# Performance work log

Measured on AMD Instinct MI355X. Metric: run time of the kernel, lower is better.

## Reference

```python
import jax, jax.numpy as jnp
import numpy as np

N = 100000      # nodes
E = 1600000     # edges (avg degree 16)
F_IN = 128      # num_features
H = 64          # hidden_dim
C = 7           # num_classes


def setup_inputs() -> dict:
    key = jax.random.key(0)
    ks = jax.random.split(key, 9)
    x = jax.random.normal(ks[0], (N, F_IN), dtype=jnp.float32)
    edge_index = jax.random.randint(ks[1], (2, E), 0, N, dtype=jnp.int32)
    s1 = 1.0 / np.sqrt(F_IN)
    s2 = 1.0 / np.sqrt(H)
    # SAGEConv1: lin_l applied to aggregated neighbors, lin_r to root
    W1l = jax.random.uniform(ks[2], (F_IN, H), jnp.float32, -s1, s1)
    W1r = jax.random.uniform(ks[3], (F_IN, H), jnp.float32, -s1, s1)
    b1 = jax.random.uniform(ks[4], (H,), jnp.float32, -s1, s1)
    # SAGEConv2
    W2l = jax.random.uniform(ks[5], (H, C), jnp.float32, -s2, s2)
    W2r = jax.random.uniform(ks[6], (H, C), jnp.float32, -s2, s2)
    b2 = jax.random.uniform(ks[7], (C,), jnp.float32, -s2, s2)
    return {"x": x, "edge_index": edge_index, "W1l": W1l, "W1r": W1r,
            "b1": b1, "W2l": W2l, "W2r": W2r, "b2": b2}


def _segment_mean(vals, idx, num_segments):
    # scatter-mean: sum messages per destination node, divide by in-degree
    sums = jax.ops.segment_sum(vals, idx, num_segments=num_segments)
    cnt = jax.ops.segment_sum(jnp.ones(idx.shape, vals.dtype), idx,
                              num_segments=num_segments)
    return sums / jnp.maximum(cnt, 1.0)[:, None]


def reference(x, edge_index, W1l, W1r, b1, W2l, W2r, b2):
    src, dst = edge_index[0], edge_index[1]
    # SAGEConv 1: mean of neighbor (src) features at each dst, plus root term
    agg1 = _segment_mean(x[src], dst, N)              # [N, F_IN]
    h = agg1 @ W1l + x @ W1r + b1                     # [N, H]
    h = jax.nn.relu(h)
    # dropout is inactive in eval mode (deterministic reference)
    # SAGEConv 2
    agg2 = _segment_mean(h[src], dst, N)              # [N, H]
    out = agg2 @ W2l + h @ W2r + b2                   # [N, C]
    return jax.nn.log_softmax(out, axis=1)
```

## Files before the change

### kernel.cpp

```cpp
#include <hip/hip_runtime.h>
#include <cstdint>
#include <cstddef>


#define CAP 64
#define BINSZ 128
#define CH 4096

typedef __attribute__((ext_vector_type(8))) short bf16x8v;
typedef __attribute__((ext_vector_type(4))) float f32x4v;
typedef __attribute__((ext_vector_type(2))) unsigned int u32x2v;

__device__ __forceinline__ float bf2f(unsigned short u) {
  return __uint_as_float(((unsigned int)u) << 16);
}
__device__ __forceinline__ unsigned short f2bf(float f) {
  unsigned int x = __float_as_uint(f);
  unsigned int r = (x + 0x7fffu + ((x >> 16) & 1u)) >> 16;
  return (unsigned short)r;
}

__device__ __forceinline__ float swap16_add(float x) {
  u32x2v p = __builtin_amdgcn_permlane16_swap(__float_as_uint(x), __float_as_uint(x), false, false);
  return __uint_as_float(p[0]) + __uint_as_float(p[1]);
}
__device__ __forceinline__ float swap32_add(float x) {
  u32x2v p = __builtin_amdgcn_permlane32_swap(__float_as_uint(x), __float_as_uint(x), false, false);
  return __uint_as_float(p[0]) + __uint_as_float(p[1]);
}

#define DPP_ROR_ADD(x, CTRL)                                                  \
  (x) = (x) + __int_as_float(__builtin_amdgcn_update_dpp(                     \
            __float_as_int(x), __float_as_int(x), (CTRL), 0xF, 0xF, false))

__global__ __launch_bounds__(256) void k_hist(const int* __restrict__ ei,
                                              int* __restrict__ hist,
                                              const float* __restrict__ W1l,
                                              const float* __restrict__ W1r,
                                              unsigned short* __restrict__ wswz,
                                              int* __restrict__ cursor,
                                              int E, int NB, int NCH) {
  const int t = threadIdx.x;
  if (blockIdx.x >= (unsigned)NCH) {
    if (blockIdx.x == (unsigned)NCH && t == 0) *cursor = 0;
    int idx = (blockIdx.x - NCH) * 256 + t;
    int j = idx & 7;
    int lane = (idx >> 3) & 63;
    int c = (idx >> 9) & 7;
    int t4 = idx >> 12;
    int kk = t4 * 32 + (lane >> 4) * 8 + j;
    int nn = c * 16 + (lane & 15);
    float v = (nn < 64) ? W1l[kk * 64 + nn] : W1r[kk * 64 + (nn - 64)];
    wswz[idx] = f2bf(v);
    return;
  }
  __shared__ int lcnt[1024];
  const int c = blockIdx.x;
  for (int i = t; i < NB; i += 256) lcnt[i] = 0;
  __syncthreads();
  const int base = c * CH;
  const int end = min(base + CH, E);
  for (int e = base + t; e < end; e += 256) {
    int d = ei[E + e];
    atomicAdd(&lcnt[d >> 7], 1);
  }
  __syncthreads();
  for (int i = t; i < NB; i += 256) hist[(size_t)i * NCH + c] = lcnt[i];
}

__global__ __launch_bounds__(256) void k_scan_gemm(
    int* __restrict__ hist, int* __restrict__ tot, int* __restrict__ binbase,
    int* __restrict__ cursor, int NB, int NCH, int nScan,
    const float* __restrict__ x, const unsigned short* __restrict__ wswz,
    const float* __restrict__ b1, unsigned short* __restrict__ xl,
    unsigned short* __restrict__ hroot, int Nn) {
  if (blockIdx.x < (unsigned)nScan) {
    const int lane = threadIdx.x & 63;
    const int bin = blockIdx.x * 4 + (threadIdx.x >> 6);
    if (bin >= NB) return;
    int* h = hist + (size_t)bin * NCH;
    int carry = 0;
    for (int base = 0; base < NCH; base += 64) {
      int i = base + lane;
      int v = (i < NCH) ? h[i] : 0;
      int incl = v;
      #pragma unroll
      for (int d = 1; d < 64; d <<= 1) {
        int t = __shfl_up(incl, d, 64);
        if (lane >= d) incl += t;
      }
      if (i < NCH) h[i] = carry + incl - v;
      carry += __shfl(incl, 63, 64);
    }
    if (lane == 0) {
      tot[bin] = carry;
      binbase[bin] = atomicAdd(cursor, carry);
    }
    return;
  }
  __shared__ unsigned short Bsw[16384];
  const int t = threadIdx.x;
  const int bid = blockIdx.x - nScan;
  {
    const uint4* src = (const uint4*)wswz;
    uint4* dst = (uint4*)Bsw;
    #pragma unroll
    for (int i = 0; i < 8; ++i) dst[t + i * 256] = src[t + i * 256];
  }
  __syncthreads();

  const int lane = t & 63;
  const int wid = t >> 6;
  const int quad = lane >> 4;
  const int m = lane & 15;
  const int rowA = bid * 64 + wid * 16 + m;
  const float* xrow = x + (size_t)min(rowA, Nn - 1) * 128;

  f32x4v acc[8];
  #pragma unroll
  for (int c = 0; c < 8; ++c) acc[c] = (f32x4v){0.f, 0.f, 0.f, 0.f};

  #pragma unroll
  for (int t4 = 0; t4 < 4; ++t4) {
    const int koff = t4 * 32 + quad * 8;
    float4 a0 = *(const float4*)(xrow + koff);
    float4 a1 = *(const float4*)(xrow + koff + 4);
    bf16x8v af;
    af[0] = (short)f2bf(a0.x); af[1] = (short)f2bf(a0.y);
    af[2] = (short)f2bf(a0.z); af[3] = (short)f2bf(a0.w);
    af[4] = (short)f2bf(a1.x); af[5] = (short)f2bf(a1.y);
    af[6] = (short)f2bf(a1.z); af[7] = (short)f2bf(a1.w);
    #pragma unroll
    for (int c = 0; c < 8; ++c) {
      const bf16x8v bf_ = *(const bf16x8v*)&Bsw[(((t4 * 8 + c) * 64 + lane)) << 3];
      acc[c] = __builtin_amdgcn_mfma_f32_16x16x32_bf16(af, bf_, acc[c], 0, 0, 0);
    }
  }

  const int rbase = bid * 64 + wid * 16 + quad * 4;
  #pragma unroll
  for (int c = 0; c < 8; ++c) {
    const int col = c * 16 + m;
    #pragma unroll
    for (int i = 0; i < 4; ++i) {
      const int r = rbase + i;
      if (r < Nn) {
        if (c < 4) xl[(size_t)r * 64 + col] = f2bf(acc[c][i]);
        else       hroot[(size_t)r * 64 + (col - 64)] = f2bf(acc[c][i] + b1[col - 64]);
      }
    }
  }
}

__global__ __launch_bounds__(256) void k_scat(const int* __restrict__ ei,
                                              const int* __restrict__ hist,
                                              const int* __restrict__ binbase,
                                              unsigned int* __restrict__ part,
                                              int E, int NB, int NCH) {
  __shared__ int lcur[1024];
  const int c = blockIdx.x, t = threadIdx.x;
  for (int i = t; i < NB; i += 256)
    lcur[i] = hist[(size_t)i * NCH + c] + binbase[i];
  __syncthreads();
  const int base = c * CH;
  const int end = min(base + CH, E);
  for (int e = base + t; e < end; e += 256) {
    int s = ei[e];
    int d = ei[E + e];
    int bin = d >> 7;
    int pos = atomicAdd(&lcur[bin], 1);
    part[pos] = (unsigned)s | ((unsigned)(d & 127) << 17);
  }
}

__global__ __launch_bounds__(256) void k_bucketB(const int* __restrict__ binbase,
                                                 const int* __restrict__ tot,
                                                 const unsigned int* __restrict__ part,
                                                 int* __restrict__ cnt,
                                                 int* __restrict__ bucket) {
  __shared__ int lbkt[BINSZ * CAP];
  __shared__ int ldeg[BINSZ];
  const int b = blockIdx.x, t = threadIdx.x;
  if (t < BINSZ) ldeg[t] = 0;
  __syncthreads();
  const int e0 = binbase[b], e1 = e0 + tot[b];
  for (int i = e0 + t; i < e1; i += 256) {
    unsigned rec = part[i];
    int loc = rec >> 17;
    int p = atomicAdd(&ldeg[loc], 1);
    if (p < CAP) lbkt[loc * CAP + p] = (int)(rec & 0x1FFFFu);
  }
  __syncthreads();
  if (t < BINSZ) cnt[b * BINSZ + t] = ldeg[t];
  const int4* s4 = (const int4*)lbkt;
  int4* d4 = (int4*)(bucket + (size_t)b * BINSZ * CAP);
  #pragma unroll 2
  for (int i = t; i < BINSZ * CAP / 4; i += 256) d4[i] = s4[i];
}

__global__ __launch_bounds__(256) void k_agg1(
    const int* __restrict__ cnt, const int* __restrict__ bucket,
    const unsigned int* __restrict__ xl32, const unsigned int* __restrict__ hroot32,
    const float* __restrict__ W2l, const float* __restrict__ W2r,
    const float* __restrict__ b2,
    float* __restrict__ hl, float* __restrict__ hr, int Nn) {
  const int lane = threadIdx.x & 63;
  const int q = lane & 15;
  const unsigned qo = 2u * q;
  const int g = lane >> 4;
  const int nw = gridDim.x * (blockDim.x >> 6);
  int n = blockIdx.x * (blockDim.x >> 6) + (threadIdx.x >> 6);
  if (n >= Nn) return;

  float wreg[4][4];
  float bcr[4];
  #pragma unroll
  for (int k = 0; k < 4; ++k) {
    const int o = (g << 2) + k;
    bcr[k] = (o >= 8 && o < 15) ? b2[o - 8] : 0.f;
    #pragma unroll
    for (int j = 0; j < 4; ++j) {
      const int kk = (q << 2) + j;
      float wv = 0.f;
      if (o < 7)                 wv = W2l[kk * 7 + o];
      else if (o >= 8 && o < 15) wv = W2r[kk * 7 + (o - 8)];
      wreg[j][k] = wv;
    }
  }

  int c  = cnt[n];
  int c1 = cnt[min(n + nw, Nn - 1)];
  int m = c < CAP ? c : CAP;
  int sidx = (lane < m) ? bucket[((unsigned)n << 6) + lane] : 0;
  if ((unsigned)sidx >= (unsigned)Nn) sidx = 0;
  uint2 hu = *(const uint2*)(hroot32 + ((unsigned)n << 5) + qo);

  while (true) {
    const int n1 = n + nw;
    const int n1c = min(n1, Nn - 1);
    const int m1 = c1 < CAP ? c1 : CAP;
    int sidx1 = (lane < m1) ? bucket[((unsigned)n1c << 6) + lane] : 0;
    uint2 hu1 = *(const uint2*)(hroot32 + ((unsigned)n1c << 5) + qo);
    int c2 = cnt[min(n1 + nw, Nn - 1)];

    float a0 = 0.f, a1 = 0.f, a2 = 0.f, a3 = 0.f;
    int i = 0;
    for (; i + 16 <= m; i += 16) {
      int rA = __shfl(sidx, i + g, 64);
      int rB = __shfl(sidx, i + 4 + g, 64);
      int rC = __shfl(sidx, i + 8 + g, 64);
      int rD = __shfl(sidx, i + 12 + g, 64);
      uint2 uA = *(const uint2*)(xl32 + (((unsigned)rA) << 5) + qo);
      uint2 uB = *(const uint2*)(xl32 + (((unsigned)rB) << 5) + qo);
      uint2 uC = *(const uint2*)(xl32 + (((unsigned)rC) << 5) + qo);
      uint2 uD = *(const uint2*)(xl32 + (((unsigned)rD) << 5) + qo);
      a0 += (__uint_as_float(uA.x << 16) + __uint_as_float(uB.x << 16))
          + (__uint_as_float(uC.x << 16) + __uint_as_float(uD.x << 16));
      a1 += (__uint_as_float(uA.x & 0xFFFF0000u) + __uint_as_float(uB.x & 0xFFFF0000u))
          + (__uint_as_float(uC.x & 0xFFFF0000u) + __uint_as_float(uD.x & 0xFFFF0000u));
      a2 += (__uint_as_float(uA.y << 16) + __uint_as_float(uB.y << 16))
          + (__uint_as_float(uC.y << 16) + __uint_as_float(uD.y << 16));
      a3 += (__uint_as_float(uA.y & 0xFFFF0000u) + __uint_as_float(uB.y & 0xFFFF0000u))
          + (__uint_as_float(uC.y & 0xFFFF0000u) + __uint_as_float(uD.y & 0xFFFF0000u));
    }
    for (; i + 8 <= m; i += 8) {
      int rA = __shfl(sidx, i + g, 64);
      int rB = __shfl(sidx, i + 4 + g, 64);
      uint2 uA = *(const uint2*)(xl32 + (((unsigned)rA) << 5) + qo);
      uint2 uB = *(const uint2*)(xl32 + (((unsigned)rB) << 5) + qo);
      a0 += __uint_as_float(uA.x << 16) + __uint_as_float(uB.x << 16);
      a1 += __uint_as_float(uA.x & 0xFFFF0000u) + __uint_as_float(uB.x & 0xFFFF0000u);
      a2 += __uint_as_float(uA.y << 16) + __uint_as_float(uB.y << 16);
      a3 += __uint_as_float(uA.y & 0xFFFF0000u) + __uint_as_float(uB.y & 0xFFFF0000u);
    }
    for (; i < m; i += 4) {
      int e = i + g;
      int r = __shfl(sidx, e & 63, 64);
      uint2 u = *(const uint2*)(xl32 + (((unsigned)r) << 5) + qo);
      if (e < m) {
        a0 += __uint_as_float(u.x << 16);
        a1 += __uint_as_float(u.x & 0xFFFF0000u);
        a2 += __uint_as_float(u.y << 16);
        a3 += __uint_as_float(u.y & 0xFFFF0000u);
      }
    }
    a0 = swap32_add(swap16_add(a0));
    a1 = swap32_add(swap16_add(a1));
    a2 = swap32_add(swap16_add(a2));
    a3 = swap32_add(swap16_add(a3));

    {
      float inv = __builtin_amdgcn_rcpf(c > 0 ? (float)c : 1.f);
      float h0 = fmaxf(fmaf(a0, inv, __uint_as_float(hu.x << 16)), 0.f);
      float h1 = fmaxf(fmaf(a1, inv, __uint_as_float(hu.x & 0xFFFF0000u)), 0.f);
      float h2 = fmaxf(fmaf(a2, inv, __uint_as_float(hu.y << 16)), 0.f);
      float h3 = fmaxf(fmaf(a3, inv, __uint_as_float(hu.y & 0xFFFF0000u)), 0.f);
      float r0 = h0 * wreg[0][0];
      r0 = fmaf(h1, wreg[1][0], r0); r0 = fmaf(h2, wreg[2][0], r0); r0 = fmaf(h3, wreg[3][0], r0);
      float r1 = h0 * wreg[0][1];
      r1 = fmaf(h1, wreg[1][1], r1); r1 = fmaf(h2, wreg[2][1], r1); r1 = fmaf(h3, wreg[3][1], r1);
      float r2 = h0 * wreg[0][2];
      r2 = fmaf(h1, wreg[1][2], r2); r2 = fmaf(h2, wreg[2][2], r2); r2 = fmaf(h3, wreg[3][2], r2);
      float r3 = h0 * wreg[0][3];
      r3 = fmaf(h1, wreg[1][3], r3); r3 = fmaf(h2, wreg[2][3], r3); r3 = fmaf(h3, wreg[3][3], r3);
      DPP_ROR_ADD(r0, 0x128); DPP_ROR_ADD(r1, 0x128);
      DPP_ROR_ADD(r2, 0x128); DPP_ROR_ADD(r3, 0x128);
      DPP_ROR_ADD(r0, 0x124); DPP_ROR_ADD(r1, 0x124);
      DPP_ROR_ADD(r2, 0x124); DPP_ROR_ADD(r3, 0x124);
      DPP_ROR_ADD(r0, 0x122); DPP_ROR_ADD(r1, 0x122);
      DPP_ROR_ADD(r2, 0x122); DPP_ROR_ADD(r3, 0x122);
      DPP_ROR_ADD(r0, 0x121); DPP_ROR_ADD(r1, 0x121);
      DPP_ROR_ADD(r2, 0x121); DPP_ROR_ADD(r3, 0x121);
      r0 += bcr[0]; r1 += bcr[1]; r2 += bcr[2]; r3 += bcr[3];
      if (q < 4) {
        float v = r0;
        if (q == 1) v = r1;
        else if (q == 2) v = r2;
        else if (q == 3) v = r3;
        float* bp = (g < 2) ? hl : hr;
        bp[((unsigned)n << 3) + ((g & 1) << 2) + q] = v;
      }
    }
    if (n1 >= Nn) break;
    n = n1; c = c1; c1 = c2; m = m1;
    sidx = ((unsigned)sidx1 >= (unsigned)Nn) ? 0 : sidx1;
    hu = hu1;
  }
}

__global__ __launch_bounds__(256) void k_out(
    const int* __restrict__ cnt, const int* __restrict__ bucket,
    const float* __restrict__ hl, const float* __restrict__ hr,
    float* __restrict__ out, int Nn) {
  const int lane = threadIdx.x & 63;
  const int c = lane & 7;
  const int sub = lane >> 3;
  const int gw = blockIdx.x * (blockDim.x >> 6) + (threadIdx.x >> 6);
  const int n = gw * 8 + sub;
  if (n >= Nn) return;
  int cn = cnt[n];
  int m = cn < CAP ? cn : CAP;
  const bool act = (c < 7);
  float acc = 0.f;
  for (int e0 = 0; e0 < m; e0 += 8) {
    int bv = (e0 + c < m) ? bucket[(size_t)n * CAP + e0 + c] : 0;
    #pragma unroll
    for (int cc = 0; cc < 8; ++cc) {
      if (e0 + cc < m) {
        int s = __shfl(bv, (lane & 56) + cc, 64);
        if ((unsigned)s >= (unsigned)Nn) s = 0;
        if (act) acc += hl[(size_t)s * 8 + c];
      }
    }
  }
  float dd = cn > 0 ? (float)cn : 1.f;
  float v = act ? (acc / dd + hr[(size_t)n * 8 + c]) : -INFINITY;
  float mx = v;
  mx = fmaxf(mx, __shfl_xor(mx, 1, 8));
  mx = fmaxf(mx, __shfl_xor(mx, 2, 8));
  mx = fmaxf(mx, __shfl_xor(mx, 4, 8));
  float ex = act ? expf(v - mx) : 0.f;
  float s2 = ex;
  s2 += __shfl_xor(s2, 1, 8);
  s2 += __shfl_xor(s2, 2, 8);
  s2 += __shfl_xor(s2, 4, 8);
  float res = v - mx - logf(s2);
  if (act) out[(size_t)n * 7 + c] = res;
}

static inline size_t alignup(size_t v) { return (v + 255) & ~(size_t)255; }

extern "C" void kernel_launch(void* const* d_in, const int* in_sizes, int n_in,
                              void* d_out, int out_size, void* d_ws, size_t ws_size,
                              hipStream_t stream) {
  const int N = in_sizes[0] / 128;
  const int E = in_sizes[1] / 2;
  const int NB = (N + BINSZ - 1) / BINSZ;
  const int Np = NB * BINSZ;
  const int NCH = (E + CH - 1) / CH;
  const int nScan = (NB + 3) / 4;

  const float* x   = (const float*)d_in[0];
  const int*   ei  = (const int*)d_in[1];
  const float* W1l = (const float*)d_in[2];
  const float* W1r = (const float*)d_in[3];
  const float* b1  = (const float*)d_in[4];
  const float* W2l = (const float*)d_in[5];
  const float* W2r = (const float*)d_in[6];
  const float* b2  = (const float*)d_in[7];
  float* out = (float*)d_out;

  char* p = (char*)d_ws;
  int* hist    = (int*)p;            p += alignup((size_t)NB * NCH * 4);
  int* tot     = (int*)p;            p += alignup((size_t)NB * 4);
  int* binbase = (int*)p;            p += alignup((size_t)(NB + 1) * 4);
  int* cursor  = (int*)p;            p += alignup(4);
  unsigned int* part = (unsigned int*)p; p += alignup((size_t)E * 4);
  int* cnt    = (int*)p;             p += alignup((size_t)Np * 4);
  int* bucket = (int*)p;             p += alignup((size_t)Np * CAP * 4);
  unsigned short* wswz = (unsigned short*)p; p += alignup((size_t)16384 * 2);
  unsigned short* xl    = (unsigned short*)p; p += alignup((size_t)N * 64 * 2);
  unsigned short* hroot = (unsigned short*)p; p += alignup((size_t)N * 64 * 2);
  float* hl  = (float*)p;            p += alignup((size_t)N * 8 * 4);
  float* hr  = (float*)p;            p += alignup((size_t)N * 8 * 4);

  dim3 b256(256);
  k_hist<<<dim3(NCH + 64), b256, 0, stream>>>(ei, hist, W1l, W1r, wswz, cursor, E, NB, NCH);
  k_scan_gemm<<<dim3(nScan + (N + 63) / 64), b256, 0, stream>>>(
      hist, tot, binbase, cursor, NB, NCH, nScan, x, wswz, b1, xl, hroot, N);
  k_scat<<<dim3(NCH), b256, 0, stream>>>(ei, hist, binbase, part, E, NB, NCH);
  k_bucketB<<<dim3(NB), b256, 0, stream>>>(binbase, tot, part, cnt, bucket);
  k_agg1<<<dim3(2048), b256, 0, stream>>>(cnt, bucket,
      (const unsigned int*)xl, (const unsigned int*)hroot,
      W2l, W2r, b2, hl, hr, N);
  const int waves_out = (N + 7) / 8;
  k_out<<<dim3((waves_out + 3) / 4), b256, 0, stream>>>(cnt, bucket, hl, hr, out, N);
}
```

Baseline: 239.2 us.

## Deepen software pipeline in layer-2 gather to prefetch next node's first neighbor chunk

Restructures the persistent per-wave node loop in the second aggregation kernel so bucket indices, root features and counts are prefetched two nodes ahead. The first 16 neighbor rows of the next node are also gathered before the current node's epilogue (matvec, DPP reduction, store). The goal is to hide gather latency behind the epilogue compute. The cost is more live registers, which may reduce occupancy, and bucket loads are now issued unconditionally for every lane.

```diff
diff --git a/kernel.cpp b/kernel.cpp
--- a/kernel.cpp
+++ b/kernel.cpp
@@ -228,23 +228,37 @@
     }
   }
 
+  int nN = n + nw;
+  int nNc = min(nN, Nn - 1);
   int c  = cnt[n];
-  int c1 = cnt[min(n + nw, Nn - 1)];
-  int m = c < CAP ? c : CAP;
-  int sidx = (lane < m) ? bucket[((unsigned)n << 6) + lane] : 0;
-  if ((unsigned)sidx >= (unsigned)Nn) sidx = 0;
-  uint2 hu = *(const uint2*)(hroot32 + ((unsigned)n << 5) + qo);
+  int cN = cnt[nNc];
+  int m  = c  < CAP ? c  : CAP;
+  int mN = cN < CAP ? cN : CAP;
+  int rawC = bucket[((unsigned)n  << 6) + lane];
+  int rawN = bucket[((unsigned)nNc << 6) + lane];
+  int sidx  = (lane < m  && (unsigned)rawC < (unsigned)Nn) ? rawC : 0;
+  int sidxN = (lane < mN && (unsigned)rawN < (unsigned)Nn) ? rawN : 0;
+  uint2 hu  = *(const uint2*)(hroot32 + ((unsigned)n   << 5) + qo);
+  uint2 huN = *(const uint2*)(hroot32 + ((unsigned)nNc << 5) + qo);
+  int cNN = cnt[min(nN + nw, Nn - 1)];
+
+  bool preflag = false;
+  uint2 pA, pB, pC, pD;
 
   while (true) {
-    const int n1 = n + nw;
-    const int n1c = min(n1, Nn - 1);
-    const int m1 = c1 < CAP ? c1 : CAP;
-    int sidx1 = (lane < m1) ? bucket[((unsigned)n1c << 6) + lane] : 0;
-    uint2 hu1 = *(const uint2*)(hroot32 + ((unsigned)n1c << 5) + qo);
-    int c2 = cnt[min(n1 + nw, Nn - 1)];
-
     float a0 = 0.f, a1 = 0.f, a2 = 0.f, a3 = 0.f;
     int i = 0;
+    if (preflag) {
+      a0 += (__uint_as_float(pA.x << 16) + __uint_as_float(pB.x << 16))
+          + (__uint_as_float(pC.x << 16) + __uint_as_float(pD.x << 16));
+      a1 += (__uint_as_float(pA.x & 0xFFFF0000u) + __uint_as_float(pB.x & 0xFFFF0000u))
+          + (__uint_as_float(pC.x & 0xFFFF0000u) + __uint_as_float(pD.x & 0xFFFF0000u));
+      a2 += (__uint_as_float(pA.y << 16) + __uint_as_float(pB.y << 16))
+          + (__uint_as_float(pC.y << 16) + __uint_as_float(pD.y << 16));
+      a3 += (__uint_as_float(pA.y & 0xFFFF0000u) + __uint_as_float(pB.y & 0xFFFF0000u))
+          + (__uint_as_float(pC.y & 0xFFFF0000u) + __uint_as_float(pD.y & 0xFFFF0000u));
+      i = 16;
+    }
     for (; i + 16 <= m; i += 16) {
       int rA = __shfl(sidx, i + g, 64);
       int rB = __shfl(sidx, i + 4 + g, 64);
@@ -288,6 +302,23 @@
     a1 = swap32_add(swap16_add(a1));
     a2 = swap32_add(swap16_add(a2));
     a3 = swap32_add(swap16_add(a3));
+
+    const int n2 = nN + nw;
+    const int n2c = min(n2, Nn - 1);
+    int raw2 = bucket[((unsigned)n2c << 6) + lane];
+    uint2 hu2 = *(const uint2*)(hroot32 + ((unsigned)n2c << 5) + qo);
+    int c3 = cnt[min(n2 + nw, Nn - 1)];
+    const bool pre = (mN >= 16);
+    if (pre) {
+      int rA = __shfl(sidxN, 0 + g, 64);
+      int rB = __shfl(sidxN, 4 + g, 64);
+      int rC = __shfl(sidxN, 8 + g, 64);
+      int rD = __shfl(sidxN, 12 + g, 64);
+      pA = *(const uint2*)(xl32 + (((unsigned)rA) << 5) + qo);
+      pB = *(const uint2*)(xl32 + (((unsigned)rB) << 5) + qo);
+      pC = *(const uint2*)(xl32 + (((unsigned)rC) << 5) + qo);
+      pD = *(const uint2*)(xl32 + (((unsigned)rD) << 5) + qo);
+    }
 
     {
       float inv = __builtin_amdgcn_rcpf(c > 0 ? (float)c : 1.f);
@@ -321,10 +352,13 @@
         bp[((unsigned)n << 3) + ((g & 1) << 2) + q] = v;
       }
     }
-    if (n1 >= Nn) break;
-    n = n1; c = c1; c1 = c2; m = m1;
-    sidx = ((unsigned)sidx1 >= (unsigned)Nn) ? 0 : sidx1;
-    hu = hu1;
+    if (nN >= Nn) break;
+    n = nN; c = cN; m = mN; sidx = sidxN; hu = huN;
+    nN = n2;
+    cN = cNN; mN = cN < CAP ? cN : CAP;
+    sidxN = (lane < mN && (unsigned)raw2 < (unsigned)Nn) ? raw2 : 0;
+    huN = hu2; cNN = c3;
+    preflag = pre;
   }
 }
 
```

Measured after the change: 234.0 us. 2.2% less time.

## Interleave bucket layout so agg lanes load neighbor indices directly as uint4

Applied to the files above, without the earlier changes.

The bucket writer now permutes each node's 64-slot neighbor list so that each 16-lane group can fetch its four neighbor indices with a single uint4 load. This replaces the per-edge cross-lane shuffles in k_agg1 with direct vector loads and a degree-specialized unrolled gather. Shared memory is zero-filled first so unused slots hold index 0 rather than garbage, which also drops the out-of-range index clamp. k_out is updated to read the permuted layout. The cost is an extra LDS clear, strided LDS reads during the bucket write, and a branchier remainder path.

```diff
diff --git a/kernel.cpp b/kernel.cpp
--- a/kernel.cpp
+++ b/kernel.cpp
@@ -181,6 +181,11 @@
   __shared__ int lbkt[BINSZ * CAP];
   __shared__ int ldeg[BINSZ];
   const int b = blockIdx.x, t = threadIdx.x;
+  {
+    int4* l4 = (int4*)lbkt;
+    #pragma unroll 2
+    for (int j = t; j < BINSZ * CAP / 4; j += 256) l4[j] = make_int4(0, 0, 0, 0);
+  }
   if (t < BINSZ) ldeg[t] = 0;
   __syncthreads();
   const int e0 = binbase[b], e1 = e0 + tot[b];
@@ -192,11 +197,62 @@
   }
   __syncthreads();
   if (t < BINSZ) cnt[b * BINSZ + t] = ldeg[t];
-  const int4* s4 = (const int4*)lbkt;
   int4* d4 = (int4*)(bucket + (size_t)b * BINSZ * CAP);
   #pragma unroll 2
-  for (int i = t; i < BINSZ * CAP / 4; i += 256) d4[i] = s4[i];
-}
+  for (int j = t; j < BINSZ * 16; j += 256) {
+    int loc = j >> 4, s = (j >> 2) & 3, g = j & 3;
+    int base = loc * 64 + s * 16 + g;
+    d4[j] = make_int4(lbkt[base], lbkt[base + 4], lbkt[base + 8], lbkt[base + 12]);
+  }
+}
+
+#define LDROW(r) (*(const uint2*)(xl32 + (((unsigned)(r)) << 5) + qo))
+#define ACC4(uA, uB, uC, uD)                                                     \
+  a0 += (__uint_as_float(uA.x << 16) + __uint_as_float(uB.x << 16))              \
+      + (__uint_as_float(uC.x << 16) + __uint_as_float(uD.x << 16));             \
+  a1 += (__uint_as_float(uA.x & 0xFFFF0000u) + __uint_as_float(uB.x & 0xFFFF0000u)) \
+      + (__uint_as_float(uC.x & 0xFFFF0000u) + __uint_as_float(uD.x & 0xFFFF0000u)); \
+  a2 += (__uint_as_float(uA.y << 16) + __uint_as_float(uB.y << 16))              \
+      + (__uint_as_float(uC.y << 16) + __uint_as_float(uD.y << 16));             \
+  a3 += (__uint_as_float(uA.y & 0xFFFF0000u) + __uint_as_float(uB.y & 0xFFFF0000u)) \
+      + (__uint_as_float(uC.y & 0xFFFF0000u) + __uint_as_float(uD.y & 0xFFFF0000u));
+#define ACC2(uA, uB)                                                             \
+  a0 += __uint_as_float(uA.x << 16) + __uint_as_float(uB.x << 16);               \
+  a1 += __uint_as_float(uA.x & 0xFFFF0000u) + __uint_as_float(uB.x & 0xFFFF0000u); \
+  a2 += __uint_as_float(uA.y << 16) + __uint_as_float(uB.y << 16);               \
+  a3 += __uint_as_float(uA.y & 0xFFFF0000u) + __uint_as_float(uB.y & 0xFFFF0000u);
+#define ACC1(u)                                                                  \
+  a0 += __uint_as_float(u.x << 16);                                              \
+  a1 += __uint_as_float(u.x & 0xFFFF0000u);                                      \
+  a2 += __uint_as_float(u.y << 16);                                              \
+  a3 += __uint_as_float(u.y & 0xFFFF0000u);
+#define STAGE(Q)                                                                 \
+  { uint2 uA = LDROW(Q.x), uB = LDROW(Q.y), uC = LDROW(Q.z), uD = LDROW(Q.w);    \
+    ACC4(uA, uB, uC, uD); }
+#define REM(Q, base)                                                             \
+  { int rem = m - (base);                                                        \
+    if (rem > 0) {                                                               \
+      if (rem >= 8) {                                                            \
+        uint2 uA = LDROW(Q.x), uB = LDROW(Q.y);                                  \
+        ACC2(uA, uB);                                                            \
+        if (rem > 8) {                                                           \
+          uint2 u = LDROW(Q.z);                                                  \
+          if ((base) + 8 + g < m) { ACC1(u); }                                   \
+          if (rem > 12) {                                                        \
+            uint2 u2 = LDROW(Q.w);                                               \
+            if ((base) + 12 + g < m) { ACC1(u2); }                               \
+          }                                                                      \
+        }                                                                        \
+      } else {                                                                   \
+        uint2 u = LDROW(Q.x);                                                    \
+        if ((base) + g < m) { ACC1(u); }                                         \
+        if (rem > 4) {                                                           \
+          uint2 u2 = LDROW(Q.y);                                                 \
+          if ((base) + 4 + g < m) { ACC1(u2); }                                  \
+        }                                                                        \
+      }                                                                          \
+    }                                                                            \
+  }
 
 __global__ __launch_bounds__(256) void k_agg1(
     const int* __restrict__ cnt, const int* __restrict__ bucket,
@@ -211,6 +267,7 @@
   const int nw = gridDim.x * (blockDim.x >> 6);
   int n = blockIdx.x * (blockDim.x >> 6) + (threadIdx.x >> 6);
   if (n >= Nn) return;
+  const uint4* exb4 = (const uint4*)bucket;
 
   float wreg[4][4];
   float bcr[4];
@@ -231,59 +288,42 @@
   int c  = cnt[n];
   int c1 = cnt[min(n + nw, Nn - 1)];
   int m = c < CAP ? c : CAP;
-  int sidx = (lane < m) ? bucket[((unsigned)n << 6) + lane] : 0;
-  if ((unsigned)sidx >= (unsigned)Nn) sidx = 0;
+  uint4 Q0 = exb4[(((unsigned)n) << 4) + g];
   uint2 hu = *(const uint2*)(hroot32 + ((unsigned)n << 5) + qo);
 
   while (true) {
     const int n1 = n + nw;
     const int n1c = min(n1, Nn - 1);
     const int m1 = c1 < CAP ? c1 : CAP;
-    int sidx1 = (lane < m1) ? bucket[((unsigned)n1c << 6) + lane] : 0;
+    uint4 Q0N = exb4[(((unsigned)n1c) << 4) + g];
     uint2 hu1 = *(const uint2*)(hroot32 + ((unsigned)n1c << 5) + qo);
     int c2 = cnt[min(n1 + nw, Nn - 1)];
 
+    const uint4* exq = exb4 + (((unsigned)n) << 4) + g;
     float a0 = 0.f, a1 = 0.f, a2 = 0.f, a3 = 0.f;
-    int i = 0;
-    for (; i + 16 <= m; i += 16) {
-      int rA = __shfl(sidx, i + g, 64);
-      int rB = __shfl(sidx, i + 4 + g, 64);
-      int rC = __shfl(sidx, i + 8 + g, 64);
-      int rD = __shfl(sidx, i + 12 + g, 64);
-      uint2 uA = *(const uint2*)(xl32 + (((unsigned)rA) << 5) + qo);
-      uint2 uB = *(const uint2*)(xl32 + (((unsigned)rB) << 5) + qo);
-      uint2 uC = *(const uint2*)(xl32 + (((unsigned)rC) << 5) + qo);
-      uint2 uD = *(const uint2*)(xl32 + (((unsigned)rD) << 5) + qo);
-      a0 += (__uint_as_float(uA.x << 16) + __uint_as_float(uB.x << 16))
-          + (__uint_as_float(uC.x << 16) + __uint_as_float(uD.x << 16));
-      a1 += (__uint_as_float(uA.x & 0xFFFF0000u) + __uint_as_float(uB.x & 0xFFFF0000u))
-          + (__uint_as_float(uC.x & 0xFFFF0000u) + __uint_as_float(uD.x & 0xFFFF0000u));
-      a2 += (__uint_as_float(uA.y << 16) + __uint_as_float(uB.y << 16))
-          + (__uint_as_float(uC.y << 16) + __uint_as_float(uD.y << 16));
-      a3 += (__uint_as_float(uA.y & 0xFFFF0000u) + __uint_as_float(uB.y & 0xFFFF0000u))
-          + (__uint_as_float(uC.y & 0xFFFF0000u) + __uint_as_float(uD.y & 0xFFFF0000u));
-    }
-    for (; i + 8 <= m; i += 8) {
-      int rA = __shfl(sidx, i + g, 64);
-      int rB = __shfl(sidx, i + 4 + g, 64);
-      uint2 uA = *(const uint2*)(xl32 + (((unsigned)rA) << 5) + qo);
-      uint2 uB = *(const uint2*)(xl32 + (((unsigned)rB) << 5) + qo);
-      a0 += __uint_as_float(uA.x << 16) + __uint_as_float(uB.x << 16);
-      a1 += __uint_as_float(uA.x & 0xFFFF0000u) + __uint_as_float(uB.x & 0xFFFF0000u);
-      a2 += __uint_as_float(uA.y << 16) + __uint_as_float(uB.y << 16);
-      a3 += __uint_as_float(uA.y & 0xFFFF0000u) + __uint_as_float(uB.y & 0xFFFF0000u);
-    }
-    for (; i < m; i += 4) {
-      int e = i + g;
-      int r = __shfl(sidx, e & 63, 64);
-      uint2 u = *(const uint2*)(xl32 + (((unsigned)r) << 5) + qo);
-      if (e < m) {
-        a0 += __uint_as_float(u.x << 16);
-        a1 += __uint_as_float(u.x & 0xFFFF0000u);
-        a2 += __uint_as_float(u.y << 16);
-        a3 += __uint_as_float(u.y & 0xFFFF0000u);
+    if (m >= 16) {
+      uint2 uA = LDROW(Q0.x), uB = LDROW(Q0.y), uC = LDROW(Q0.z), uD = LDROW(Q0.w);
+      uint4 Q1;
+      if (m > 16) Q1 = exq[4];
+      ACC4(uA, uB, uC, uD);
+      if (m >= 32) {
+        STAGE(Q1);
+        if (m >= 48) {
+          uint4 Q2 = exq[8];
+          STAGE(Q2);
+          if (m >= 64) { uint4 Q3 = exq[12]; STAGE(Q3); }
+          else if (m > 48) { uint4 Q3 = exq[12]; REM(Q3, 48); }
+        } else if (m > 32) {
+          uint4 Q2 = exq[8];
+          REM(Q2, 32);
+        }
+      } else if (m > 16) {
+        REM(Q1, 16);
       }
-    }
+    } else {
+      REM(Q0, 0);
+    }
+
     a0 = swap32_add(swap16_add(a0));
     a1 = swap32_add(swap16_add(a1));
     a2 = swap32_add(swap16_add(a2));
@@ -323,8 +363,7 @@
     }
     if (n1 >= Nn) break;
     n = n1; c = c1; c1 = c2; m = m1;
-    sidx = ((unsigned)sidx1 >= (unsigned)Nn) ? 0 : sidx1;
-    hu = hu1;
+    Q0 = Q0N; hu = hu1;
   }
 }
 
@@ -343,7 +382,9 @@
   const bool act = (c < 7);
   float acc = 0.f;
   for (int e0 = 0; e0 < m; e0 += 8) {
-    int bv = (e0 + c < m) ? bucket[(size_t)n * CAP + e0 + c] : 0;
+    int e = e0 + c;
+    int exi = (e & ~15) | ((e & 3) << 2) | ((e >> 2) & 3);
+    int bv = (e < m) ? bucket[(size_t)n * CAP + exi] : 0;
     #pragma unroll
     for (int cc = 0; cc < 8; ++cc) {
       if (e0 + cc < m) {
```

Result: no change. 237.9 us (-0.6%).
